# Kernel tuning notes

Measured on AMD Instinct MI355X. Metric: run time of the kernel, lower is better.

Reference implementation:

```python
import jax, jax.numpy as jnp
import numpy as np

HEADS = 8

def group_conv1x1(x, w, heads):
    # x: (B, Cin, H, W); w: (Cout, Cin//heads, 1, 1) grouped 1x1 conv, no bias
    B, Cin, H, W = x.shape
    Cout = w.shape[0]
    xg = x.reshape(B, heads, Cin // heads, H * W)
    wg = w[:, :, 0, 0].reshape(heads, Cout // heads, Cin // heads)
    out = jnp.einsum('hoc,bhcl->bhol', wg, xg)
    return out.reshape(B, Cout, H, W)

def sine_pe(d_model, length):
    # standard transformer sin/cos encoding, laid out as (d_model, length)
    pos = jnp.arange(length, dtype=jnp.float32)
    i = jnp.arange(0, d_model, 2, dtype=jnp.float32)
    div = jnp.exp(-(jnp.log(10000.0)) * i / d_model)
    ang = div[:, None] * pos[None, :]            # (d/2, L)
    pe = jnp.zeros((d_model, length), dtype=jnp.float32)
    pe = pe.at[0::2].set(jnp.sin(ang)).at[1::2].set(jnp.cos(ang))
    return pe

def setup_inputs() -> dict:
    key = jax.random.key(0)
    k0, k1, k2, k3 = jax.random.split(key, 4)
    B, Cin, H, W = 16, 256, 32, 32
    Cout, heads = 256, HEADS
    fan_out = Cout  # kaiming_normal fan_out for 1x1 conv = Cout*1*1
    std = np.sqrt(2.0 / fan_out)
    x = jax.random.normal(k0, (B, Cin, H, W), dtype=jnp.float32)
    wq = jax.random.normal(k1, (Cout, Cin // heads, 1, 1), dtype=jnp.float32) * std
    wk = jax.random.normal(k2, (Cout, Cin // heads, 1, 1), dtype=jnp.float32) * std
    wv = jax.random.normal(k3, (Cout, Cin // heads, 1, 1), dtype=jnp.float32) * std
    return {"x": x, "wq": wq, "wk": wk, "wv": wv}

def reference(x, wq, wk, wv):
    B, Cin, H, W = x.shape
    Cout = wq.shape[0]
    heads = HEADS
    dh = Cout // heads
    L = H * W

    q = group_conv1x1(x, wq, heads)              # (B, Cout, H, W)
    k = group_conv1x1(x, wk, heads)
    v = group_conv1x1(x, wv, heads)

    # sine positional encoding added to keys over flattened spatial positions
    k = k.reshape(B, Cout, L) + sine_pe(Cout, L)[None]

    q = q.reshape(B, heads, dh, L)               # (B, h, dh, L)
    k = k.reshape(B, heads, dh, L)
    v = v.reshape(B, heads, dh, L)

    scores = jnp.einsum('bhdq,bhdk->bhqk', q, k)  # (B, h, L, L) -- no sqrt(d) scaling, as in source
    attn = jax.nn.softmax(scores, axis=-1)
    out = jnp.einsum('bhqk,bhdk->bhdq', attn, v)  # (B, h, dh, L)
    return out.reshape(B, Cout, H, W)
```

## Files before the change

### kernel.cpp

```cpp
#include <hip/hip_runtime.h>

#define LL   1024
#define LOG2E 1.44269504088896340736f
#define SMEM_BYTES (131072 + 20480 + 32)

typedef unsigned int       uint;
typedef unsigned short     ushort;
typedef unsigned long long ull;

typedef __attribute__((ext_vector_type(8)))  __bf16          bf16x8;
typedef __attribute__((ext_vector_type(8)))  unsigned short  u16x8;
typedef __attribute__((ext_vector_type(4)))  unsigned short  u16x4;
typedef __attribute__((ext_vector_type(2)))  uint            ui32x2;
typedef __attribute__((ext_vector_type(4)))  uint            ui32x4;
typedef __attribute__((ext_vector_type(4)))  float           f32x4;
typedef __attribute__((ext_vector_type(16))) float           f32x16;

static __device__ __forceinline__ ushort f2bf(float f){
  union {float f; uint u;} v; v.f = f;
  uint u = v.u + 0x7fffu + ((v.u >> 16) & 1u);
  return (ushort)(u >> 16);
}
static __device__ __forceinline__ uint pack2(float a, float b){
  return (uint)f2bf(a) | ((uint)f2bf(b) << 16);
}
static __device__ __forceinline__ uint packtrunc(float a, float b){
  union {float f; uint u;} x, y; x.f = a; y.f = b;
  return __builtin_amdgcn_perm(y.u, x.u, 0x07060302u);
}
static __device__ __forceinline__ bf16x8 ld_frag(const ushort* p){
  u16x8 t = *(const u16x8*)p;
  return __builtin_bit_cast(bf16x8, t);
}
static __device__ __forceinline__ bf16x8 cvt8(const float* p){
  float4 f0 = *(const float4*)p, f1 = *(const float4*)(p + 4);
  u16x8 t;
  t[0]=f2bf(f0.x); t[1]=f2bf(f0.y); t[2]=f2bf(f0.z); t[3]=f2bf(f0.w);
  t[4]=f2bf(f1.x); t[5]=f2bf(f1.y); t[6]=f2bf(f1.z); t[7]=f2bf(f1.w);
  return __builtin_bit_cast(bf16x8, t);
}

static __device__ __forceinline__ void plane32_swap(uint& a, uint& b){
  asm("v_permlane32_swap_b32 %0, %1" : "+v"(a), "+v"(b));
}

static __device__ __forceinline__ void attn_tile(
    f32x16& O, float& rs, bf16x8 q0, bf16x8 q1,
    const bf16x8* kf, const bf16x8* vf)
{
  f32x16 zz = {};
  f32x16 st0 = __builtin_amdgcn_mfma_f32_32x32x16_bf16(kf[0], q0, zz,  0,0,0);
  st0        = __builtin_amdgcn_mfma_f32_32x32x16_bf16(kf[1], q1, st0, 0,0,0);
  f32x16 st1 = __builtin_amdgcn_mfma_f32_32x32x16_bf16(kf[2], q0, zz,  0,0,0);
  st1        = __builtin_amdgcn_mfma_f32_32x32x16_bf16(kf[3], q1, st1, 0,0,0);

  uint pr0[8], pr1[8];
  float s0 = 0.f, s1 = 0.f, s2 = 0.f, s3 = 0.f;
  #pragma unroll
  for (int zi = 0; zi < 8; ++zi){
    float a0 = __builtin_amdgcn_exp2f(st0[2*zi]);
    float a1 = __builtin_amdgcn_exp2f(st0[2*zi+1]);
    float b0 = __builtin_amdgcn_exp2f(st1[2*zi]);
    float b1 = __builtin_amdgcn_exp2f(st1[2*zi+1]);
    s0 += a0; s1 += a1; s2 += b0; s3 += b1;
    pr0[zi] = packtrunc(a0, a1);
    pr1[zi] = packtrunc(b0, b1);
  }
  rs += (s0 + s1) + (s2 + s3);

  #pragma unroll
  for (int c = 0; c < 4; ++c){
    const uint* pr = (c < 2) ? pr0 : pr1;
    const int g0 = 4*(c & 1);
    uint p0 = pr[g0+0], p1 = pr[g0+1], p2 = pr[g0+2], p3 = pr[g0+3];
    plane32_swap(p0, p2);
    plane32_swap(p1, p3);
    ui32x4 pb; pb[0]=p0; pb[1]=p1; pb[2]=p2; pb[3]=p3;
    O = __builtin_amdgcn_mfma_f32_32x32x16_bf16(
          vf[c], __builtin_bit_cast(bf16x8, pb), O, 0,0,0);
  }
}

__global__ __launch_bounds__(512, 1) void fused_kernel(
    const void* __restrict__ xr,
    const void* __restrict__ wqr,
    const void* __restrict__ wkr,
    const void* __restrict__ wvr,
    void* __restrict__ out)
{
  extern __shared__ __align__(16) char smem[];
  ushort* Ks = (ushort*)smem;
  ushort* Vs = Ks + 32768;
  uint (*xbuf)[20] = (uint (*)[20])(Vs + 32768);
  int* cnt = (int*)(smem + 131072 + 20480);

  const int bh   = blockIdx.x;
  const int qh   = blockIdx.y;
  const int tid  = threadIdx.x;
  const int wave = tid >> 6;
  const int lane = tid & 63;
  const int l16  = lane & 15;
  const int quad = lane >> 4;
  const int q32  = lane & 31;
  const int h    = lane >> 5;

  bool is_bf;
  {
    uint w = ((const uint*)xr)[tid & 255];
    uint e = (w >> 7) & 0xFFu;
    ull b = __ballot((e >= 118u) && (e <= 132u));
    if (lane == 0) cnt[wave] = __popcll(b);
    __syncthreads();
    int s = 0;
    #pragma unroll
    for (int i = 0; i < 8; ++i) s += cnt[i];
    is_bf = s > 256;
  }

  bf16x8 bwk[2], bwv[2], aq[2];
  #pragma unroll
  for (int nh = 0; nh < 2; ++nh){
    const int row = (bh & 7)*32 + nh*16 + l16;
    if (is_bf){
      bwk[nh] = ld_frag((const ushort*)wkr + (size_t)row*32 + quad*8);
      bwv[nh] = ld_frag((const ushort*)wvr + (size_t)row*32 + quad*8);
    } else {
      bwk[nh] = cvt8((const float*)wkr + (size_t)row*32 + quad*8);
      bwv[nh] = cvt8((const float*)wvr + (size_t)row*32 + quad*8);
    }
  }
  {
    const int row = (bh & 7)*32 + q32;
    if (is_bf){
      aq[0] = ld_frag((const ushort*)wqr + (size_t)row*32 + h*8);
      aq[1] = ld_frag((const ushort*)wqr + (size_t)row*32 + 16 + h*8);
    } else {
      aq[0] = cvt8((const float*)wqr + (size_t)row*32 + h*8);
      aq[1] = cvt8((const float*)wqr + (size_t)row*32 + 16 + h*8);
    }
  }

  float fA[2], fB[2];
  #pragma unroll
  for (int nh = 0; nh < 2; ++nh){
    const int c0 = (bh & 7)*32 + nh*16 + quad*4;
    fA[nh] = __expf(-0.03597789207f * (float)c0);
    fB[nh] = __expf(-0.03597789207f * (float)(c0 + 2));
  }

  const int myoc = 4*qh + (wave >> 1);
  bf16x8 bq[2][2];

  const int cp = tid & 15, lg = tid >> 4;

  uint dw[4];
  {
    const size_t rb = (size_t)(bh*32 + 2*cp)*LL + lg*4;
    if (is_bf){
      u16x4 e = *(const u16x4*)((const ushort*)xr + rb);
      u16x4 o = *(const u16x4*)((const ushort*)xr + rb + LL);
      #pragma unroll
      for (int j = 0; j < 4; ++j) dw[j] = (uint)e[j] | ((uint)o[j] << 16);
    } else {
      const float* xf = (const float*)xr;
      float4 e0 = *(const float4*)(xf + rb);
      float4 o0 = *(const float4*)(xf + rb + LL);
      dw[0]=pack2(e0.x,o0.x); dw[1]=pack2(e0.y,o0.y);
      dw[2]=pack2(e0.z,o0.z); dw[3]=pack2(e0.w,o0.w);
    }
  }

  for (int lc = 0; lc < 8; ++lc){
    uint (*xs)[20] = xbuf + (lc & 1)*128;
    #pragma unroll
    for (int j = 0; j < 4; ++j) xs[lg*4 + j][cp] = dw[j];
    __syncthreads();

    if (lc < 7){
      const size_t rb = (size_t)(bh*32 + 2*cp)*LL + (size_t)(lc+1)*128 + lg*4;
      if (is_bf){
        u16x4 e = *(const u16x4*)((const ushort*)xr + rb);
        u16x4 o = *(const u16x4*)((const ushort*)xr + rb + LL);
        #pragma unroll
        for (int j = 0; j < 4; ++j) dw[j] = (uint)e[j] | ((uint)o[j] << 16);
      } else {
        const float* xf = (const float*)xr;
        float4 e0 = *(const float4*)(xf + rb);
        float4 o0 = *(const float4*)(xf + rb + LL);
        dw[0]=pack2(e0.x,o0.x); dw[1]=pack2(e0.y,o0.y);
        dw[2]=pack2(e0.z,o0.z); dw[3]=pack2(e0.w,o0.w);
      }
    }

    bf16x8 ax = __builtin_bit_cast(bf16x8,
                  *(const ui32x4*)&xs[wave*16 + l16][quad*4]);

    const f32x4 z = {0.f,0.f,0.f,0.f};
    f32x4 dk[2], dv[2];
    #pragma unroll
    for (int nh = 0; nh < 2; ++nh){
      dk[nh] = __builtin_amdgcn_mfma_f32_16x16x32_bf16(bwk[nh], ax, z, 0,0,0);
      dv[nh] = __builtin_amdgcn_mfma_f32_16x16x32_bf16(ax, bwv[nh], z, 0,0,0);
    }

    {
      const int kl = lc*128 + wave*16 + l16;
      const int kbase = (kl >> 6)*2048 + ((kl >> 5) & 1)*1024
                      + (quad >> 1)*256 + (kl & 31)*8 + (quad & 1)*4;
      #pragma unroll
      for (int nh = 0; nh < 2; ++nh){
        const float aa = fA[nh] * (float)kl, ab = fB[nh] * (float)kl;
        const float k0 = (dk[nh][0] + __sinf(aa)) * LOG2E;
        const float k1 = (dk[nh][1] + __cosf(aa)) * LOG2E;
        const float k2 = (dk[nh][2] + __sinf(ab)) * LOG2E;
        const float k3 = (dk[nh][3] + __cosf(ab)) * LOG2E;
        ui32x2 ww = { pack2(k0, k1), pack2(k2, k3) };
        *(ui32x2*)&Ks[kbase + nh*512] = ww;
      }
    }
    {
      const int vl = lc*128 + wave*16 + quad*4;
      const int vbase = (vl >> 6)*2048 + (wave & 3)*512
                      + (quad >> 1)*256 + (quad & 1)*4;
      #pragma unroll
      for (int nh = 0; nh < 2; ++nh){
        ui32x2 ww = { pack2(dv[nh][0], dv[nh][1]),
                      pack2(dv[nh][2], dv[nh][3]) };
        *(ui32x2*)&Vs[vbase + (nh*16 + l16)*8] = ww;
      }
    }

    if (lc == myoc){
      const int xbase = (wave & 1)*64;
      #pragma unroll
      for (int qt2 = 0; qt2 < 2; ++qt2){
        const int xrow = xbase + qt2*32 + q32;
        bf16x8 bxl = __builtin_bit_cast(bf16x8, *(const ui32x4*)&xs[xrow][h*4]);
        bf16x8 bxh = __builtin_bit_cast(bf16x8, *(const ui32x4*)&xs[xrow][8 + h*4]);
        f32x16 zz = {};
        f32x16 dq = __builtin_amdgcn_mfma_f32_32x32x16_bf16(aq[0], bxl, zz, 0,0,0);
        dq        = __builtin_amdgcn_mfma_f32_32x32x16_bf16(aq[1], bxh, dq, 0,0,0);
        uint prq[8];
        #pragma unroll
        for (int zi = 0; zi < 8; ++zi) prq[zi] = pack2(dq[2*zi], dq[2*zi+1]);
        #pragma unroll
        for (int hf = 0; hf < 2; ++hf){
          const int g0 = 4*hf;
          uint p0 = prq[g0+0], p1 = prq[g0+1], p2 = prq[g0+2], p3 = prq[g0+3];
          plane32_swap(p0, p2);
          plane32_swap(p1, p3);
          ui32x4 pb; pb[0]=p0; pb[1]=p1; pb[2]=p2; pb[3]=p3;
          bq[qt2][hf] = __builtin_bit_cast(bf16x8, pb);
        }
      }
    }
  }
  __syncthreads();

  const ushort* kb = Ks + h*256 + q32*8;
  const ushort* vb = Vs + h*256 + q32*8;

  f32x16 O0 = {}, O1 = {};
  float rs0 = 0.f, rs1 = 0.f;

  bf16x8 kf[4], vf[4];
  #pragma unroll
  for (int i = 0; i < 4; ++i){
    kf[i] = ld_frag(kb + i*512);
    vf[i] = ld_frag(vb + i*512);
  }

  for (int kt = 0; kt < 16; ++kt){
    const int nkt = (kt + 1) & 15;
    bf16x8 nk[4], nv[4];
    #pragma unroll
    for (int i = 0; i < 4; ++i){
      nk[i] = ld_frag(kb + nkt*2048 + i*512);
      nv[i] = ld_frag(vb + nkt*2048 + i*512);
    }
    attn_tile(O0, rs0, bq[0][0], bq[0][1], kf, vf);
    attn_tile(O1, rs1, bq[1][0], bq[1][1], kf, vf);
    #pragma unroll
    for (int i = 0; i < 4; ++i){ kf[i] = nk[i]; vf[i] = nv[i]; }
  }

  rs0 += __shfl_xor(rs0, 32);
  rs1 += __shfl_xor(rs1, 32);
  const float inv0 = 1.f / rs0, inv1 = 1.f / rs1;

  const int qg0 = qh*512 + wave*64 + q32;
  #pragma unroll
  for (int reg = 0; reg < 16; ++reg){
    const int d = (reg & 3) + 8*(reg >> 2) + 4*h;
    const size_t o0 = ((size_t)(bh*32 + d))*LL + qg0;
    if (is_bf){
      ((ushort*)out)[o0]      = f2bf(O0[reg] * inv0);
      ((ushort*)out)[o0 + 32] = f2bf(O1[reg] * inv1);
    } else {
      ((float*)out)[o0]      = O0[reg] * inv0;
      ((float*)out)[o0 + 32] = O1[reg] * inv1;
    }
  }
}

extern "C" void kernel_launch(void* const* d_in, const int* in_sizes, int n_in,
                              void* d_out, int out_size, void* d_ws, size_t ws_size,
                              hipStream_t stream) {
  (void)d_ws; (void)ws_size; (void)in_sizes; (void)n_in; (void)out_size;
  static bool inited = false;
  if (!inited){
    hipFuncSetAttribute(reinterpret_cast<const void*>(fused_kernel),
                        hipFuncAttributeMaxDynamicSharedMemorySize, SMEM_BYTES);
    inited = true;
  }
  fused_kernel<<<dim3(128, 2), 512, SMEM_BYTES, stream>>>(
      d_in[0], d_in[1], d_in[2], d_in[3], d_out);
}
```

Measured before the change: 102.7 us.

## Double block to 1024 threads, splitting K/V projection and halving per-wave query tiles

Launches 1024 threads per block instead of 512. Waves 0-7 compute the K projection and waves 8-15 compute V, and only the upper waves stage x into shared memory. Each wave now handles one 32-query tile instead of two, which doubles wave-level parallelism in the attention loop. The cost is that every wave still reloads all of K/V from shared memory, so LDS traffic per query doubles, and there is more barrier overhead with 16 waves.

Result: no change. 102.7 us (-0.0%).

```diff
diff --git a/kernel.cpp b/kernel.cpp
--- a/kernel.cpp
+++ b/kernel.cpp
@@ -2,7 +2,7 @@
 
 #define LL   1024
 #define LOG2E 1.44269504088896340736f
-#define SMEM_BYTES (131072 + 20480 + 32)
+#define SMEM_BYTES (131072 + 20480 + 64)
 
 typedef unsigned int       uint;
 typedef unsigned short     ushort;
@@ -81,7 +81,7 @@
   }
 }
 
-__global__ __launch_bounds__(512, 1) void fused_kernel(
+__global__ __launch_bounds__(1024, 1) void fused_kernel(
     const void* __restrict__ xr,
     const void* __restrict__ wqr,
     const void* __restrict__ wkr,
@@ -103,6 +103,7 @@
   const int quad = lane >> 4;
   const int q32  = lane & 31;
   const int h    = lane >> 5;
+  const int cw   = wave & 7;
 
   bool is_bf;
   {
@@ -113,21 +114,17 @@
     __syncthreads();
     int s = 0;
     #pragma unroll
-    for (int i = 0; i < 8; ++i) s += cnt[i];
-    is_bf = s > 256;
-  }
-
-  bf16x8 bwk[2], bwv[2], aq[2];
+    for (int i = 0; i < 16; ++i) s += cnt[i];
+    is_bf = s > 512;
+  }
+
+  const void* wpr = (wave < 8) ? wkr : wvr;
+  bf16x8 bwp[2], aq[2];
   #pragma unroll
   for (int nh = 0; nh < 2; ++nh){
     const int row = (bh & 7)*32 + nh*16 + l16;
-    if (is_bf){
-      bwk[nh] = ld_frag((const ushort*)wkr + (size_t)row*32 + quad*8);
-      bwv[nh] = ld_frag((const ushort*)wvr + (size_t)row*32 + quad*8);
-    } else {
-      bwk[nh] = cvt8((const float*)wkr + (size_t)row*32 + quad*8);
-      bwv[nh] = cvt8((const float*)wvr + (size_t)row*32 + quad*8);
-    }
+    if (is_bf) bwp[nh] = ld_frag((const ushort*)wpr + (size_t)row*32 + quad*8);
+    else       bwp[nh] = cvt8((const float*)wpr + (size_t)row*32 + quad*8);
   }
   {
     const int row = (bh & 7)*32 + q32;
@@ -148,13 +145,14 @@
     fB[nh] = __expf(-0.03597789207f * (float)(c0 + 2));
   }
 
-  const int myoc = 4*qh + (wave >> 1);
-  bf16x8 bq[2][2];
-
-  const int cp = tid & 15, lg = tid >> 4;
+  const int myoc = 4*qh + (wave >> 2);
+  bf16x8 bq[2];
+
+  const int sid = tid & 511;
+  const int cp = sid & 15, lg = sid >> 4;
 
   uint dw[4];
-  {
+  if (wave >= 8){
     const size_t rb = (size_t)(bh*32 + 2*cp)*LL + lg*4;
     if (is_bf){
       u16x4 e = *(const u16x4*)((const ushort*)xr + rb);
@@ -172,11 +170,13 @@
 
   for (int lc = 0; lc < 8; ++lc){
     uint (*xs)[20] = xbuf + (lc & 1)*128;
-    #pragma unroll
-    for (int j = 0; j < 4; ++j) xs[lg*4 + j][cp] = dw[j];
+    if (wave >= 8){
+      #pragma unroll
+      for (int j = 0; j < 4; ++j) xs[lg*4 + j][cp] = dw[j];
+    }
     __syncthreads();
 
-    if (lc < 7){
+    if (wave >= 8 && lc < 7){
       const size_t rb = (size_t)(bh*32 + 2*cp)*LL + (size_t)(lc+1)*128 + lg*4;
       if (is_bf){
         u16x4 e = *(const u16x4*)((const ushort*)xr + rb);
@@ -193,18 +193,15 @@
     }
 
     bf16x8 ax = __builtin_bit_cast(bf16x8,
-                  *(const ui32x4*)&xs[wave*16 + l16][quad*4]);
-
+                  *(const ui32x4*)&xs[cw*16 + l16][quad*4]);
     const f32x4 z = {0.f,0.f,0.f,0.f};
-    f32x4 dk[2], dv[2];
-    #pragma unroll
-    for (int nh = 0; nh < 2; ++nh){
-      dk[nh] = __builtin_amdgcn_mfma_f32_16x16x32_bf16(bwk[nh], ax, z, 0,0,0);
-      dv[nh] = __builtin_amdgcn_mfma_f32_16x16x32_bf16(ax, bwv[nh], z, 0,0,0);
-    }
-
-    {
-      const int kl = lc*128 + wave*16 + l16;
+
+    if (wave < 8){
+      f32x4 dk[2];
+      #pragma unroll
+      for (int nh = 0; nh < 2; ++nh)
+        dk[nh] = __builtin_amdgcn_mfma_f32_16x16x32_bf16(bwp[nh], ax, z, 0,0,0);
+      const int kl = lc*128 + cw*16 + l16;
       const int kbase = (kl >> 6)*2048 + ((kl >> 5) & 1)*1024
                       + (quad >> 1)*256 + (kl & 31)*8 + (quad & 1)*4;
       #pragma unroll
@@ -217,10 +214,13 @@
         ui32x2 ww = { pack2(k0, k1), pack2(k2, k3) };
         *(ui32x2*)&Ks[kbase + nh*512] = ww;
       }
-    }
-    {
-      const int vl = lc*128 + wave*16 + quad*4;
-      const int vbase = (vl >> 6)*2048 + (wave & 3)*512
+    } else {
+      f32x4 dv[2];
+      #pragma unroll
+      for (int nh = 0; nh < 2; ++nh)
+        dv[nh] = __builtin_amdgcn_mfma_f32_16x16x32_bf16(ax, bwp[nh], z, 0,0,0);
+      const int vl = lc*128 + cw*16 + quad*4;
+      const int vbase = (vl >> 6)*2048 + (cw & 3)*512
                       + (quad >> 1)*256 + (quad & 1)*4;
       #pragma unroll
       for (int nh = 0; nh < 2; ++nh){
@@ -231,27 +231,23 @@
     }
 
     if (lc == myoc){
-      const int xbase = (wave & 1)*64;
-      #pragma unroll
-      for (int qt2 = 0; qt2 < 2; ++qt2){
-        const int xrow = xbase + qt2*32 + q32;
-        bf16x8 bxl = __builtin_bit_cast(bf16x8, *(const ui32x4*)&xs[xrow][h*4]);
-        bf16x8 bxh = __builtin_bit_cast(bf16x8, *(const ui32x4*)&xs[xrow][8 + h*4]);
-        f32x16 zz = {};
-        f32x16 dq = __builtin_amdgcn_mfma_f32_32x32x16_bf16(aq[0], bxl, zz, 0,0,0);
-        dq        = __builtin_amdgcn_mfma_f32_32x32x16_bf16(aq[1], bxh, dq, 0,0,0);
-        uint prq[8];
-        #pragma unroll
-        for (int zi = 0; zi < 8; ++zi) prq[zi] = pack2(dq[2*zi], dq[2*zi+1]);
-        #pragma unroll
-        for (int hf = 0; hf < 2; ++hf){
-          const int g0 = 4*hf;
-          uint p0 = prq[g0+0], p1 = prq[g0+1], p2 = prq[g0+2], p3 = prq[g0+3];
-          plane32_swap(p0, p2);
-          plane32_swap(p1, p3);
-          ui32x4 pb; pb[0]=p0; pb[1]=p1; pb[2]=p2; pb[3]=p3;
-          bq[qt2][hf] = __builtin_bit_cast(bf16x8, pb);
-        }
+      const int xrow = (wave & 3)*32 + q32;
+      bf16x8 bxl = __builtin_bit_cast(bf16x8, *(const ui32x4*)&xs[xrow][h*4]);
+      bf16x8 bxh = __builtin_bit_cast(bf16x8, *(const ui32x4*)&xs[xrow][8 + h*4]);
+      f32x16 zz = {};
+      f32x16 dq = __builtin_amdgcn_mfma_f32_32x32x16_bf16(aq[0], bxl, zz, 0,0,0);
+      dq        = __builtin_amdgcn_mfma_f32_32x32x16_bf16(aq[1], bxh, dq, 0,0,0);
+      uint prq[8];
+      #pragma unroll
+      for (int zi = 0; zi < 8; ++zi) prq[zi] = pack2(dq[2*zi], dq[2*zi+1]);
+      #pragma unroll
+      for (int hf = 0; hf < 2; ++hf){
+        const int g0 = 4*hf;
+        uint p0 = prq[g0+0], p1 = prq[g0+1], p2 = prq[g0+2], p3 = prq[g0+3];
+        plane32_swap(p0, p2);
+        plane32_swap(p1, p3);
+        ui32x4 pb; pb[0]=p0; pb[1]=p1; pb[2]=p2; pb[3]=p3;
+        bq[hf] = __builtin_bit_cast(bf16x8, pb);
       }
     }
   }
@@ -260,8 +256,8 @@
   const ushort* kb = Ks + h*256 + q32*8;
   const ushort* vb = Vs + h*256 + q32*8;
 
-  f32x16 O0 = {}, O1 = {};
-  float rs0 = 0.f, rs1 = 0.f;
+  f32x16 O = {};
+  float rs = 0.f;
 
   bf16x8 kf[4], vf[4];
   #pragma unroll
@@ -278,28 +274,22 @@
       nk[i] = ld_frag(kb + nkt*2048 + i*512);
       nv[i] = ld_frag(vb + nkt*2048 + i*512);
     }
-    attn_tile(O0, rs0, bq[0][0], bq[0][1], kf, vf);
-    attn_tile(O1, rs1, bq[1][0], bq[1][1], kf, vf);
+    attn_tile(O, rs, bq[0], bq[1], kf, vf);
     #pragma unroll
     for (int i = 0; i < 4; ++i){ kf[i] = nk[i]; vf[i] = nv[i]; }
   }
 
-  rs0 += __shfl_xor(rs0, 32);
-  rs1 += __shfl_xor(rs1, 32);
-  const float inv0 = 1.f / rs0, inv1 = 1.f / rs1;
-
-  const int qg0 = qh*512 + wave*64 + q32;
+  rs += __shfl_xor(rs, 32);
+  const float inv = 1.f / rs;
+
+  const int qg0 = qh*512 + wave*32 + q32;
   #pragma unroll
   for (int reg = 0; reg < 16; ++reg){
     const int d = (reg & 3) + 8*(reg >> 2) + 4*h;
-    const size_t o0 = ((size_t)(bh*32 + d))*LL + qg0;
-    if (is_bf){
-      ((ushort*)out)[o0]      = f2bf(O0[reg] * inv0);
-      ((ushort*)out)[o0 + 32] = f2bf(O1[reg] * inv1);
-    } else {
-      ((float*)out)[o0]      = O0[reg] * inv0;
-      ((float*)out)[o0 + 32] = O1[reg] * inv1;
-    }
+    const float v = O[reg] * inv;
+    const size_t off = ((size_t)(bh*32 + d))*LL + qg0;
+    if (is_bf) ((ushort*)out)[off] = f2bf(v);
+    else       ((float*)out)[off]  = v;
   }
 }
 
@@ -313,6 +303,6 @@
                         hipFuncAttributeMaxDynamicSharedMemorySize, SMEM_BYTES);
     inited = true;
   }
-  fused_kernel<<<dim3(128, 2), 512, SMEM_BYTES, stream>>>(
+  fused_kernel<<<dim3(128, 2), 1024, SMEM_BYTES, stream>>>(
       d_in[0], d_in[1], d_in[2], d_in[3], d_out);
 }
```
